# Kernel tuning notes

Hardware: AMD Instinct MI355X
Metric: run time of the kernel (lower is better)

## Reference

```python
import jax, jax.numpy as jnp
import numpy as np

B, L, HEADS, D_HEAD = 2, 2048, 16, 64
D_MODEL = HEADS * D_HEAD            # 1024
D_BI = D_MODEL * 4 // 2             # 2048 (bilinear GLU width)
D_PROJ = D_MODEL * 3 + 2 * D_BI
DEPTH = 0                           # block depth < 2 -> token shift active
NEG_INF = -1e10


def _ln(x, g, b, eps=1e-5):
    m = jnp.mean(x, axis=-1, keepdims=True)
    v = jnp.var(x, axis=-1, keepdims=True)
    return (x - m) * jax.lax.rsqrt(v + eps) * g + b


def _shift(x, n):
    # F.pad(x, (0,0,n,-n)): shift along seq dim by n, zero-fill at front
    return jnp.pad(x, ((0, 0), (n, 0), (0, 0)))[:, : x.shape[1], :]


def setup_inputs() -> dict:
    key = jax.random.key(0)
    ks = jax.random.split(key, 3)
    x = jax.random.normal(ks[0], (B, L, D_MODEL), jnp.float32)
    w_in = jax.random.normal(ks[1], (D_MODEL, D_PROJ), jnp.float32) * (D_MODEL ** -0.5)
    # note: torch init zeros out_proj; we use small random weights so backward is non-trivial
    w_out = jax.random.normal(ks[2], (D_MODEL + D_BI, D_MODEL), jnp.float32) * 0.02
    slopes = jnp.concatenate([2.0 ** jnp.linspace(0.0, -6.0, HEADS // 2),
                              jnp.zeros(HEADS - HEADS // 2)]).astype(jnp.float32)
    return {
        "x": x,
        "in_ln_g": jnp.ones(D_MODEL, jnp.float32), "in_ln_b": jnp.zeros(D_MODEL, jnp.float32),
        "mid_ln_g": jnp.ones(D_PROJ, jnp.float32), "mid_ln_b": jnp.zeros(D_PROJ, jnp.float32),
        "out_ln_g": jnp.ones(D_MODEL, jnp.float32), "out_ln_b": jnp.zeros(D_MODEL, jnp.float32),
        "w_in": w_in, "w_out": w_out, "slopes": slopes,
    }


def reference(x, in_ln_g, in_ln_b, mid_ln_g, mid_ln_b, out_ln_g, out_ln_b, w_in, w_out, slopes):
    b, l, d = x.shape
    x = _ln(x, in_ln_g, in_ln_b)
    if DEPTH < 2:
        x = jnp.concatenate([
            _shift(x[..., : d // 4], 1),
            x[..., d // 4: d - d // 8],
            _shift(x[..., d - d // 8:], 2),
        ], axis=-1)
    h = _ln(x @ w_in, mid_ln_g, mid_ln_b)
    q, k, v, p1, p2 = jnp.split(h, [D_MODEL, 2 * D_MODEL, 3 * D_MODEL, 3 * D_MODEL + D_BI], axis=-1)
    to_heads = lambda t: t.reshape(b, l, HEADS, D_HEAD).transpose(0, 2, 1, 3)  # b h l d
    q, k, v = to_heads(q), to_heads(k), to_heads(v)
    logits = jnp.einsum('bhid,bhjd->bhij', q, k) * (D_HEAD ** -0.5)
    pos = jnp.arange(l)
    alibi = pos[None, None, None, :].astype(logits.dtype) * slopes[None, :, None, None]
    causal = jnp.where(pos[:, None] >= pos[None, :], 0.0, NEG_INF).astype(logits.dtype)
    a = jax.nn.softmax(logits + alibi + causal, axis=-1)
    o = jnp.einsum('bhij,bhjd->bhid', a, v).transpose(0, 2, 1, 3).reshape(b, l, d)
    return _ln(jnp.concatenate([o, p1 * p2], axis=-1) @ w_out, out_ln_g, out_ln_b)
```

## Files before the change

kernel.cpp:

```cpp
#include <hip/hip_runtime.h>

#define B_ 2
#define L_ 2048
#define HEADS_ 16
#define DH_ 64
#define DM_ 1024
#define DBI_ 2048
#define DPROJ_ 7168
#define NTOK (B_*L_)
#define DCAT (DM_ + DBI_)

typedef __bf16 bf16;
typedef __attribute__((ext_vector_type(8))) __bf16 bf16x8;
typedef __attribute__((ext_vector_type(4))) float floatx4;

typedef __attribute__((address_space(1))) const void gptr_t;
typedef __attribute__((address_space(3))) void lptr_t;

__device__ __forceinline__ void g2l16(const void* g, void* l) {
    __builtin_amdgcn_global_load_lds((gptr_t*)g, (lptr_t*)l, 16, 0, 0);
}

__global__ __launch_bounds__(256) void transpose_both(const float* __restrict__ w_in,
                                                      const float* __restrict__ w_out,
                                                      bf16* __restrict__ w_inT,
                                                      bf16* __restrict__ w_outT) {
    __shared__ float tile[32][33];
    int l = blockIdx.x;
    const float* in; bf16* outp; int R, C, bx, by;
    if (l < 7168) { in = w_in;  outp = w_inT;  R = DM_;  C = DPROJ_; bx = l % 224; by = l / 224; }
    else { l -= 7168; in = w_out; outp = w_outT; R = DCAT; C = DM_;   bx = l % 32;  by = l / 32; }
    int c0 = bx * 32, r0 = by * 32;
    int x = threadIdx.x & 31, y = threadIdx.x >> 5;
    for (int i = 0; i < 32; i += 8)
        tile[y + i][x] = in[(size_t)(r0 + y + i) * C + (c0 + x)];
    __syncthreads();
    for (int i = 0; i < 32; i += 8)
        outp[(size_t)(c0 + y + i) * R + (r0 + x)] = (bf16)tile[x][y + i];
}

__global__ __launch_bounds__(256) void ln_shift(const float* __restrict__ x,
                                                const float* __restrict__ g,
                                                const float* __restrict__ bb,
                                                bf16* __restrict__ xs) {
    int tok = blockIdx.x;
    int b = tok / L_, l = tok % L_;
    const float* row = x + (size_t)tok * DM_;
    float vals[4];
    float s = 0.f, s2 = 0.f;
    for (int i = 0; i < 4; i++) {
        float v = row[threadIdx.x + i * 256];
        vals[i] = v; s += v; s2 += v * v;
    }
    __shared__ float red[2][4];
    for (int o = 32; o; o >>= 1) { s += __shfl_xor(s, o); s2 += __shfl_xor(s2, o); }
    int w = threadIdx.x >> 6;
    if ((threadIdx.x & 63) == 0) { red[0][w] = s; red[1][w] = s2; }
    __syncthreads();
    s  = red[0][0] + red[0][1] + red[0][2] + red[0][3];
    s2 = red[1][0] + red[1][1] + red[1][2] + red[1][3];
    float mean = s * (1.f / DM_);
    float var  = s2 * (1.f / DM_) - mean * mean;
    float rstd = rsqrtf(var + 1e-5f);
    for (int i = 0; i < 4; i++) {
        int c = threadIdx.x + i * 256;
        float y = (vals[i] - mean) * rstd * g[c] + bb[c];
        int shift = (c < 256) ? 1 : ((c >= 896) ? 2 : 0);
        int dl = l + shift;
        if (dl < L_) xs[((size_t)b * L_ + dl) * DM_ + c] = (bf16)y;
        if (l == 0 && shift) {
            xs[((size_t)b * L_ + 0) * DM_ + c] = (bf16)0.f;
            if (shift == 2) xs[((size_t)b * L_ + 1) * DM_ + c] = (bf16)0.f;
        }
    }
}

__global__ __launch_bounds__(256, 2) void gemm1_k(const bf16* __restrict__ A,
                                                  const bf16* __restrict__ Bt,
                                                  bf16* __restrict__ C) {
    const int K = DM_, N = DPROJ_;
    int lin = blockIdx.x;
    int chunk = lin >> 7, within = lin & 127;
    int m0 = (within >> 3) * 256;
    int n0 = (chunk * 8 + (within & 7)) * 128;
    __shared__ bf16 As[2][256 * 32];
    __shared__ bf16 Bs[2][128 * 32];
    int t = threadIdx.x, lane = t & 63, wave = t >> 6;
    int c = lane & 15, quad = lane >> 4;
    int wm = wave * 64;
    auto stage = [&](int k0, int bsel) {
        #pragma unroll
        for (int s = 0; s < 4; s++) {
            int f = s * 256 + t;
            int row = f >> 2, kp = (f & 3) * 8;
            g2l16(A + (size_t)(m0 + row) * K + k0 + kp, &As[bsel][f * 8]);
        }
        #pragma unroll
        for (int s = 0; s < 2; s++) {
            int f = s * 256 + t;
            int row = f >> 2, kp = (f & 3) * 8;
            g2l16(Bt + (size_t)(n0 + row) * K + k0 + kp, &Bs[bsel][f * 8]);
        }
    };
    floatx4 acc[4][8] = {};
    stage(0, 0);
    int buf = 0;
    for (int k0 = 0; k0 < K; k0 += 32) {
        __syncthreads();
        if (k0 + 32 < K) stage(k0 + 32, buf ^ 1);
        bf16x8 af[4], bfr[8];
        #pragma unroll
        for (int i = 0; i < 4; i++)
            af[i] = *(const bf16x8*)&As[buf][(wm + i * 16 + c) * 32 + quad * 8];
        #pragma unroll
        for (int j = 0; j < 8; j++)
            bfr[j] = *(const bf16x8*)&Bs[buf][(j * 16 + c) * 32 + quad * 8];
        #pragma unroll
        for (int i = 0; i < 4; i++)
            #pragma unroll
            for (int j = 0; j < 8; j++)
                acc[i][j] = __builtin_amdgcn_mfma_f32_16x16x32_bf16(af[i], bfr[j], acc[i][j], 0, 0, 0);
        buf ^= 1;
    }
    #pragma unroll
    for (int i = 0; i < 4; i++)
        #pragma unroll
        for (int j = 0; j < 8; j++)
            #pragma unroll
            for (int r = 0; r < 4; r++) {
                int row = m0 + wm + i * 16 + quad * 4 + r;
                int col = n0 + j * 16 + c;
                C[(size_t)row * N + col] = (bf16)acc[i][j][r];
            }
}

__global__ __launch_bounds__(256) void gemm2_sk(const bf16* __restrict__ A,
                                                const bf16* __restrict__ Bt,
                                                float* __restrict__ P) {
    const int ldA = DCAT, N = DM_;
    int m0 = blockIdx.x * 128, n0 = blockIdx.y * 128, kz = blockIdx.z;
    const bf16* Ak = A + kz * 1024;
    const bf16* Btk = Bt + kz * 1024;
    float* C = P + (size_t)kz * NTOK * DM_;
    __shared__ bf16 As[2][128 * 32];
    __shared__ bf16 Bs[2][128 * 32];
    int t = threadIdx.x, lane = t & 63, wave = t >> 6;
    int c = lane & 15, quad = lane >> 4;
    int wm = (wave >> 1) * 64, wn = (wave & 1) * 64;
    auto stage = [&](int k0, int bsel) {
        #pragma unroll
        for (int s = 0; s < 2; s++) {
            int f = s * 256 + t;
            int row = f >> 2, kp = (f & 3) * 8;
            g2l16(Ak + (size_t)(m0 + row) * ldA + k0 + kp, &As[bsel][f * 8]);
            g2l16(Btk + (size_t)(n0 + row) * ldA + k0 + kp, &Bs[bsel][f * 8]);
        }
    };
    floatx4 acc[4][4] = {};
    stage(0, 0);
    int buf = 0;
    for (int k0 = 0; k0 < 1024; k0 += 32) {
        __syncthreads();
        if (k0 + 32 < 1024) stage(k0 + 32, buf ^ 1);
        bf16x8 af[4], bfr[4];
        #pragma unroll
        for (int i = 0; i < 4; i++)
            af[i] = *(const bf16x8*)&As[buf][(wm + i * 16 + c) * 32 + quad * 8];
        #pragma unroll
        for (int j = 0; j < 4; j++)
            bfr[j] = *(const bf16x8*)&Bs[buf][(wn + j * 16 + c) * 32 + quad * 8];
        #pragma unroll
        for (int i = 0; i < 4; i++)
            #pragma unroll
            for (int j = 0; j < 4; j++)
                acc[i][j] = __builtin_amdgcn_mfma_f32_16x16x32_bf16(af[i], bfr[j], acc[i][j], 0, 0, 0);
        buf ^= 1;
    }
    #pragma unroll
    for (int i = 0; i < 4; i++)
        #pragma unroll
        for (int j = 0; j < 4; j++)
            #pragma unroll
            for (int r = 0; r < 4; r++) {
                int row = m0 + wm + i * 16 + quad * 4 + r;
                int col = n0 + wn + j * 16 + c;
                C[(size_t)row * N + col] = acc[i][j][r];
            }
}

__global__ __launch_bounds__(256) void mid_ln_fused(const bf16* __restrict__ h,
                                                    const float* __restrict__ g,
                                                    const float* __restrict__ bb,
                                                    bf16* __restrict__ Qp,
                                                    bf16* __restrict__ Kp,
                                                    bf16* __restrict__ Vn,
                                                    bf16* __restrict__ A2) {
    int tok = blockIdx.x;
    int b = tok >> 11, l = tok & 2047;
    size_t base = (size_t)tok * DPROJ_;
    int t = threadIdx.x;
    float v[28];
    float s = 0.f, s2 = 0.f;
    for (int i = 0; i < 28; i++) {
        v[i] = (float)h[base + t + i * 256];
        s += v[i]; s2 += v[i] * v[i];
    }
    __shared__ float red[2][4];
    for (int o = 32; o; o >>= 1) { s += __shfl_xor(s, o); s2 += __shfl_xor(s2, o); }
    int w = t >> 6;
    if ((t & 63) == 0) { red[0][w] = s; red[1][w] = s2; }
    __syncthreads();
    s  = red[0][0] + red[0][1] + red[0][2] + red[0][3];
    s2 = red[1][0] + red[1][1] + red[1][2] + red[1][3];
    float mean = s * (1.f / DPROJ_);
    float var  = s2 * (1.f / DPROJ_) - mean * mean;
    float rstd = rsqrtf(var + 1e-5f);
    #pragma unroll
    for (int i = 0; i < 28; i++) {
        int c = t + i * 256;
        v[i] = (v[i] - mean) * rstd * g[c] + bb[c];
    }
    #pragma unroll
    for (int i = 0; i < 12; i++) {
        int c = t + i * 256;
        int sec = c >> 10;
        int cc = c & 1023;
        int hh = cc >> 6, d = cc & 63;
        size_t idx = (((size_t)b * HEADS_ + hh) * L_ + l) * DH_ + d;
        bf16* dst = (sec == 0) ? Qp : (sec == 1) ? Kp : Vn;
        dst[idx] = (bf16)v[i];
    }
    #pragma unroll
    for (int i = 12; i < 20; i++) {
        int c = t + i * 256;
        A2[(size_t)tok * DCAT + DM_ + (c - 3 * DM_)] = (bf16)(v[i] * v[i + 8]);
    }
}

__global__ __launch_bounds__(256) void vt_pack(const bf16* __restrict__ Vn,
                                               bf16* __restrict__ Vt) {
    __shared__ bf16 tile[32][33];
    int bh = blockIdx.z;
    const bf16* in = Vn + (size_t)bh * L_ * DH_;
    bf16* out = Vt + (size_t)bh * DH_ * L_;
    int l0 = blockIdx.x * 32, d0 = blockIdx.y * 32;
    int x = threadIdx.x & 31, y = threadIdx.x >> 5;
    for (int i = 0; i < 32; i += 8)
        tile[y + i][x] = in[(size_t)(l0 + y + i) * DH_ + d0 + x];
    __syncthreads();
    for (int i = 0; i < 32; i += 8)
        out[(size_t)(d0 + y + i) * L_ + l0 + x] = tile[x][y + i];
}

__global__ __launch_bounds__(256, 4) void attn4(const bf16* __restrict__ Qp,
                                                const bf16* __restrict__ Kp,
                                                const bf16* __restrict__ Vt,
                                                const float* __restrict__ slopes,
                                                bf16* __restrict__ A2) {
    int hd = blockIdx.y, b = blockIdx.z;
    int lin = blockIdx.x + 32 * blockIdx.y + 512 * blockIdx.z;
    int xr = blockIdx.x;
    int qt = ((lin >> 8) & 1) ? (31 - xr) : xr;
    int q0 = qt * 64;
    int t = threadIdx.x, lane = t & 63, wave = t >> 6;
    int quad = lane >> 4, c = lane & 15;
    __shared__ bf16 Ks[2 * 64 * 32];
    __shared__ bf16 Vs[2 * 64 * 32];
    __shared__ bf16 Ps[4][16 * 72];
    int bh = b * HEADS_ + hd;
    const bf16* Qb = Qp + (size_t)bh * L_ * DH_;
    const bf16* Kb = Kp + (size_t)bh * L_ * DH_;
    const bf16* Vb = Vt + (size_t)bh * DH_ * L_;
    const float LOG2E = 1.44269504f;
    float slopeL2 = slopes[hd] * LOG2E;
    const float qscale = 0.125f * LOG2E;

    bf16x8 qf[2];
    int qrow = q0 + wave * 16 + c;
    qf[0] = *(const bf16x8*)(Qb + (size_t)qrow * DH_ + quad * 8);
    qf[1] = *(const bf16x8*)(Qb + (size_t)qrow * DH_ + 32 + quad * 8);
    floatx4 accO[4] = {};
    float lsum[4];
    float mrow[4];
    int i_row0 = q0 + wave * 16 + quad * 4;
    #pragma unroll
    for (int r = 0; r < 4; r++) {
        lsum[r] = 0.f;
        mrow[r] = slopeL2 * (float)(i_row0 + r) + 20.0f;
    }

    int row = t >> 2, kp = (t & 3) * 8;
    bf16* pw = &Ps[wave][0];
    bf16* pwr = pw + (quad * 4) * 72 + c;
    for (int j0 = 0; j0 <= q0; j0 += 64) {
        #pragma unroll
        for (int s = 0; s < 2; s++) {
            g2l16(Kb + (size_t)(j0 + row) * DH_ + s * 32 + kp, &Ks[(s * 256 + t) * 8]);
            g2l16(Vb + (size_t)row * L_ + j0 + s * 32 + kp, &Vs[(s * 256 + t) * 8]);
        }
        __syncthreads();

        bool diag = (j0 == q0);
        #pragma unroll
        for (int nt = 0; nt < 4; nt++) {
            floatx4 sacc = {};
            bf16x8 kf0 = *(const bf16x8*)&Ks[(nt * 16 + c) * 32 + quad * 8];
            bf16x8 kf1 = *(const bf16x8*)&Ks[2048 + (nt * 16 + c) * 32 + quad * 8];
            sacc = __builtin_amdgcn_mfma_f32_16x16x32_bf16(qf[0], kf0, sacc, 0, 0, 0);
            sacc = __builtin_amdgcn_mfma_f32_16x16x32_bf16(qf[1], kf1, sacc, 0, 0, 0);
            int j = j0 + nt * 16 + c;
            float aj = slopeL2 * (float)j;
            #pragma unroll
            for (int r = 0; r < 4; r++) {
                float p = exp2f(fmaf(sacc[r], qscale, aj) - mrow[r]);
                if (diag) p = (j <= i_row0 + r) ? p : 0.f;
                lsum[r] += p;
                pwr[r * 72 + nt * 16] = (bf16)p;
            }
        }
        bf16x8 pf0 = *(const bf16x8*)&pw[c * 72 + quad * 8];
        bf16x8 pf1 = *(const bf16x8*)&pw[c * 72 + 32 + quad * 8];
        #pragma unroll
        for (int nt = 0; nt < 4; nt++) {
            bf16x8 vf0 = *(const bf16x8*)&Vs[(nt * 16 + c) * 32 + quad * 8];
            bf16x8 vf1 = *(const bf16x8*)&Vs[2048 + (nt * 16 + c) * 32 + quad * 8];
            accO[nt] = __builtin_amdgcn_mfma_f32_16x16x32_bf16(pf0, vf0, accO[nt], 0, 0, 0);
            accO[nt] = __builtin_amdgcn_mfma_f32_16x16x32_bf16(pf1, vf1, accO[nt], 0, 0, 0);
        }
        __syncthreads();
    }
    #pragma unroll
    for (int r = 0; r < 4; r++) {
        float l = lsum[r];
        l += __shfl_xor(l, 1);
        l += __shfl_xor(l, 2);
        l += __shfl_xor(l, 4);
        l += __shfl_xor(l, 8);
        lsum[r] = 1.f / l;
    }
    #pragma unroll
    for (int r = 0; r < 4; r++) {
        size_t orow = (size_t)b * L_ + q0 + wave * 16 + quad * 4 + r;
        #pragma unroll
        for (int nt = 0; nt < 4; nt++)
            A2[orow * DCAT + hd * DH_ + nt * 16 + c] = (bf16)(accO[nt][r] * lsum[r]);
    }
}

__global__ __launch_bounds__(256) void out_ln3(const float* __restrict__ P,
                                               const float* __restrict__ g,
                                               const float* __restrict__ bb,
                                               float* __restrict__ out) {
    size_t base = (size_t)blockIdx.x * DM_;
    const size_t stride = (size_t)NTOK * DM_;
    float v[4];
    float s = 0.f, s2 = 0.f;
    for (int i = 0; i < 4; i++) {
        size_t idx = base + threadIdx.x + i * 256;
        v[i] = P[idx] + P[idx + stride] + P[idx + 2 * stride];
        s += v[i]; s2 += v[i] * v[i];
    }
    __shared__ float red[2][4];
    for (int o = 32; o; o >>= 1) { s += __shfl_xor(s, o); s2 += __shfl_xor(s2, o); }
    int w = threadIdx.x >> 6;
    if ((threadIdx.x & 63) == 0) { red[0][w] = s; red[1][w] = s2; }
    __syncthreads();
    s  = red[0][0] + red[0][1] + red[0][2] + red[0][3];
    s2 = red[1][0] + red[1][1] + red[1][2] + red[1][3];
    float mean = s * (1.f / DM_);
    float var  = s2 * (1.f / DM_) - mean * mean;
    float rstd = rsqrtf(var + 1e-5f);
    for (int i = 0; i < 4; i++) {
        int c = threadIdx.x + i * 256;
        out[base + c] = (v[i] - mean) * rstd * g[c] + bb[c];
    }
}

extern "C" void kernel_launch(void* const* d_in, const int* in_sizes, int n_in,
                              void* d_out, int out_size, void* d_ws, size_t ws_size,
                              hipStream_t stream) {
    const float* x     = (const float*)d_in[0];
    const float* in_g  = (const float*)d_in[1];
    const float* in_b  = (const float*)d_in[2];
    const float* mid_g = (const float*)d_in[3];
    const float* mid_b = (const float*)d_in[4];
    const float* out_g = (const float*)d_in[5];
    const float* out_b = (const float*)d_in[6];
    const float* w_in  = (const float*)d_in[7];
    const float* w_out = (const float*)d_in[8];
    const float* slopes = (const float*)d_in[9];
    float* out = (float*)d_out;

    char* ws = (char*)d_ws;
    size_t off = 0;
    auto alloc = [&](size_t n) { char* p = ws + off; off += (n + 255) & ~(size_t)255; return p; };
    bf16* w_inT  = (bf16*)alloc((size_t)DPROJ_ * DM_ * 2);
    bf16* w_outT = (bf16*)alloc((size_t)DM_ * DCAT * 2);
    bf16* xs     = (bf16*)alloc((size_t)NTOK * DM_ * 2);
    bf16* h      = (bf16*)alloc((size_t)NTOK * DPROJ_ * 2);
    bf16* A2     = (bf16*)alloc((size_t)NTOK * DCAT * 2);
    bf16* Qp     = (bf16*)alloc((size_t)NTOK * DM_ * 2);
    bf16* Kp     = (bf16*)alloc((size_t)NTOK * DM_ * 2);
    bf16* Vn     = (bf16*)alloc((size_t)NTOK * DM_ * 2);
    bf16* Vt = xs;
    float* P = (float*)h;

    hipLaunchKernelGGL(transpose_both, dim3(7168 + 3072), dim3(256), 0, stream,
                       w_in, w_out, w_inT, w_outT);
    hipLaunchKernelGGL(ln_shift, dim3(NTOK), dim3(256), 0, stream, x, in_g, in_b, xs);
    hipLaunchKernelGGL(gemm1_k, dim3(896), dim3(256), 0, stream, xs, w_inT, h);
    hipLaunchKernelGGL(mid_ln_fused, dim3(NTOK), dim3(256), 0, stream, h, mid_g, mid_b,
                       Qp, Kp, Vn, A2);
    hipLaunchKernelGGL(vt_pack, dim3(L_ / 32, DH_ / 32, B_ * HEADS_), dim3(256), 0, stream, Vn, Vt);
    hipLaunchKernelGGL(attn4, dim3(32, HEADS_, B_), dim3(256), 0, stream, Qp, Kp, Vt, slopes, A2);
    hipLaunchKernelGGL(gemm2_sk, dim3(NTOK / 128, DM_ / 128, 3), dim3(256), 0, stream,
                       A2, w_outT, P);
    hipLaunchKernelGGL(out_ln3, dim3(NTOK), dim3(256), 0, stream, P, out_g, out_b, out);
}
```

Baseline: 317.3 us.

## Vectorize layernorm kernels and raise GEMM occupancy hints

Rewrites the input, mid and output layernorm kernels to use 16-byte vector loads and stores (float4 / bf16x8) in place of scalar per-element accesses. The mid layernorm kernel remaps threads so each one handles contiguous 8-element chunks, with a split between threads below and above 128 to route Q/K/V and bilinear products. Launch-bound minimum block counts for the two GEMMs are also raised, which pushes the compiler toward fewer registers and risks spills. These changes target memory-bound elementwise kernels and GEMM occupancy.

```diff
diff --git a/kernel.cpp b/kernel.cpp
--- a/kernel.cpp
+++ b/kernel.cpp
@@ -11,6 +11,7 @@
 #define DCAT (DM_ + DBI_)
 
 typedef __bf16 bf16;
+typedef __attribute__((ext_vector_type(4))) __bf16 bf16x4;
 typedef __attribute__((ext_vector_type(8))) __bf16 bf16x8;
 typedef __attribute__((ext_vector_type(4))) float floatx4;
 
@@ -44,38 +45,40 @@
                                                 const float* __restrict__ bb,
                                                 bf16* __restrict__ xs) {
     int tok = blockIdx.x;
-    int b = tok / L_, l = tok % L_;
-    const float* row = x + (size_t)tok * DM_;
-    float vals[4];
-    float s = 0.f, s2 = 0.f;
-    for (int i = 0; i < 4; i++) {
-        float v = row[threadIdx.x + i * 256];
-        vals[i] = v; s += v; s2 += v * v;
-    }
+    int b = tok >> 11, l = tok & 2047;
+    int t = threadIdx.x;
+    float4 v = ((const float4*)(x + (size_t)tok * DM_))[t];
+    float s = v.x + v.y + v.z + v.w;
+    float s2 = v.x * v.x + v.y * v.y + v.z * v.z + v.w * v.w;
     __shared__ float red[2][4];
     for (int o = 32; o; o >>= 1) { s += __shfl_xor(s, o); s2 += __shfl_xor(s2, o); }
-    int w = threadIdx.x >> 6;
-    if ((threadIdx.x & 63) == 0) { red[0][w] = s; red[1][w] = s2; }
+    int w = t >> 6;
+    if ((t & 63) == 0) { red[0][w] = s; red[1][w] = s2; }
     __syncthreads();
     s  = red[0][0] + red[0][1] + red[0][2] + red[0][3];
     s2 = red[1][0] + red[1][1] + red[1][2] + red[1][3];
     float mean = s * (1.f / DM_);
     float var  = s2 * (1.f / DM_) - mean * mean;
     float rstd = rsqrtf(var + 1e-5f);
-    for (int i = 0; i < 4; i++) {
-        int c = threadIdx.x + i * 256;
-        float y = (vals[i] - mean) * rstd * g[c] + bb[c];
-        int shift = (c < 256) ? 1 : ((c >= 896) ? 2 : 0);
-        int dl = l + shift;
-        if (dl < L_) xs[((size_t)b * L_ + dl) * DM_ + c] = (bf16)y;
-        if (l == 0 && shift) {
-            xs[((size_t)b * L_ + 0) * DM_ + c] = (bf16)0.f;
-            if (shift == 2) xs[((size_t)b * L_ + 1) * DM_ + c] = (bf16)0.f;
-        }
-    }
-}
-
-__global__ __launch_bounds__(256, 2) void gemm1_k(const bf16* __restrict__ A,
+    int c = t * 4;
+    float4 gg = ((const float4*)g)[t];
+    float4 bv = ((const float4*)bb)[t];
+    bf16x4 y;
+    y[0] = (bf16)((v.x - mean) * rstd * gg.x + bv.x);
+    y[1] = (bf16)((v.y - mean) * rstd * gg.y + bv.y);
+    y[2] = (bf16)((v.z - mean) * rstd * gg.z + bv.z);
+    y[3] = (bf16)((v.w - mean) * rstd * gg.w + bv.w);
+    int shift = (c < 256) ? 1 : ((c >= 896) ? 2 : 0);
+    int dl = l + shift;
+    if (dl < L_) *(bf16x4*)&xs[((size_t)b * L_ + dl) * DM_ + c] = y;
+    if (l == 0 && shift) {
+        bf16x4 z = {};
+        *(bf16x4*)&xs[((size_t)b * L_) * DM_ + c] = z;
+        if (shift == 2) *(bf16x4*)&xs[((size_t)b * L_ + 1) * DM_ + c] = z;
+    }
+}
+
+__global__ __launch_bounds__(256, 3) void gemm1_k(const bf16* __restrict__ A,
                                                   const bf16* __restrict__ Bt,
                                                   bf16* __restrict__ C) {
     const int K = DM_, N = DPROJ_;
@@ -134,9 +137,9 @@
             }
 }
 
-__global__ __launch_bounds__(256) void gemm2_sk(const bf16* __restrict__ A,
-                                                const bf16* __restrict__ Bt,
-                                                float* __restrict__ P) {
+__global__ __launch_bounds__(256, 4) void gemm2_sk(const bf16* __restrict__ A,
+                                                   const bf16* __restrict__ Bt,
+                                                   float* __restrict__ P) {
     const int ldA = DCAT, N = DM_;
     int m0 = blockIdx.x * 128, n0 = blockIdx.y * 128, kz = blockIdx.z;
     const bf16* Ak = A + kz * 1024;
@@ -197,13 +200,18 @@
                                                     bf16* __restrict__ A2) {
     int tok = blockIdx.x;
     int b = tok >> 11, l = tok & 2047;
-    size_t base = (size_t)tok * DPROJ_;
+    const bf16x8* hrow = (const bf16x8*)(h + (size_t)tok * DPROJ_);
     int t = threadIdx.x;
-    float v[28];
+    int nch = (t < 128) ? 4 : 3;
+    float v[4][8];
     float s = 0.f, s2 = 0.f;
-    for (int i = 0; i < 28; i++) {
-        v[i] = (float)h[base + t + i * 256];
-        s += v[i]; s2 += v[i] * v[i];
+    for (int i = 0; i < nch; i++) {
+        bf16x8 hv = hrow[t + i * 256];
+        #pragma unroll
+        for (int j = 0; j < 8; j++) {
+            float f = (float)hv[j];
+            v[i][j] = f; s += f; s2 += f * f;
+        }
     }
     __shared__ float red[2][4];
     for (int o = 32; o; o >>= 1) { s += __shfl_xor(s, o); s2 += __shfl_xor(s2, o); }
@@ -215,25 +223,40 @@
     float mean = s * (1.f / DPROJ_);
     float var  = s2 * (1.f / DPROJ_) - mean * mean;
     float rstd = rsqrtf(var + 1e-5f);
-    #pragma unroll
-    for (int i = 0; i < 28; i++) {
-        int c = t + i * 256;
-        v[i] = (v[i] - mean) * rstd * g[c] + bb[c];
-    }
-    #pragma unroll
-    for (int i = 0; i < 12; i++) {
-        int c = t + i * 256;
-        int sec = c >> 10;
-        int cc = c & 1023;
+    for (int i = 0; i < nch; i++) {
+        int c = (t + i * 256) * 8;
+        float4 g0 = *(const float4*)&g[c],  g1 = *(const float4*)&g[c + 4];
+        float4 b0 = *(const float4*)&bb[c], b1 = *(const float4*)&bb[c + 4];
+        v[i][0] = (v[i][0] - mean) * rstd * g0.x + b0.x;
+        v[i][1] = (v[i][1] - mean) * rstd * g0.y + b0.y;
+        v[i][2] = (v[i][2] - mean) * rstd * g0.z + b0.z;
+        v[i][3] = (v[i][3] - mean) * rstd * g0.w + b0.w;
+        v[i][4] = (v[i][4] - mean) * rstd * g1.x + b1.x;
+        v[i][5] = (v[i][5] - mean) * rstd * g1.y + b1.y;
+        v[i][6] = (v[i][6] - mean) * rstd * g1.z + b1.z;
+        v[i][7] = (v[i][7] - mean) * rstd * g1.w + b1.w;
+    }
+    bf16x8 o;
+    {
+        int cc = (t < 128) ? t * 8 : (t - 128) * 8;
         int hh = cc >> 6, d = cc & 63;
-        size_t idx = (((size_t)b * HEADS_ + hh) * L_ + l) * DH_ + d;
-        bf16* dst = (sec == 0) ? Qp : (sec == 1) ? Kp : Vn;
-        dst[idx] = (bf16)v[i];
-    }
-    #pragma unroll
-    for (int i = 12; i < 20; i++) {
-        int c = t + i * 256;
-        A2[(size_t)tok * DCAT + DM_ + (c - 3 * DM_)] = (bf16)(v[i] * v[i + 8]);
+        #pragma unroll
+        for (int j = 0; j < 8; j++) o[j] = (bf16)v[0][j];
+        bf16* dst = (t < 128) ? Qp : Kp;
+        *(bf16x8*)&dst[(((size_t)b * HEADS_ + hh) * L_ + l) * DH_ + d] = o;
+    }
+    if (t < 128) {
+        int cc = t * 8, hh = cc >> 6, d = cc & 63;
+        #pragma unroll
+        for (int j = 0; j < 8; j++) o[j] = (bf16)v[1][j];
+        *(bf16x8*)&Vn[(((size_t)b * HEADS_ + hh) * L_ + l) * DH_ + d] = o;
+        #pragma unroll
+        for (int j = 0; j < 8; j++) o[j] = (bf16)(v[2][j] * v[3][j]);
+        *(bf16x8*)&A2[(size_t)tok * DCAT + DM_ + t * 8 + 1024] = o;
+    } else {
+        #pragma unroll
+        for (int j = 0; j < 8; j++) o[j] = (bf16)(v[1][j] * v[2][j]);
+        *(bf16x8*)&A2[(size_t)tok * DCAT + DM_ + (t - 128) * 8] = o;
     }
 }
 
@@ -353,27 +376,33 @@
                                                float* __restrict__ out) {
     size_t base = (size_t)blockIdx.x * DM_;
     const size_t stride = (size_t)NTOK * DM_;
-    float v[4];
-    float s = 0.f, s2 = 0.f;
-    for (int i = 0; i < 4; i++) {
-        size_t idx = base + threadIdx.x + i * 256;
-        v[i] = P[idx] + P[idx + stride] + P[idx + 2 * stride];
-        s += v[i]; s2 += v[i] * v[i];
-    }
+    int t = threadIdx.x;
+    float4 a = *(const float4*)&P[base + t * 4];
+    float4 b1 = *(const float4*)&P[base + stride + t * 4];
+    float4 c1 = *(const float4*)&P[base + 2 * stride + t * 4];
+    float4 v;
+    v.x = a.x + b1.x + c1.x; v.y = a.y + b1.y + c1.y;
+    v.z = a.z + b1.z + c1.z; v.w = a.w + b1.w + c1.w;
+    float s = v.x + v.y + v.z + v.w;
+    float s2 = v.x * v.x + v.y * v.y + v.z * v.z + v.w * v.w;
     __shared__ float red[2][4];
     for (int o = 32; o; o >>= 1) { s += __shfl_xor(s, o); s2 += __shfl_xor(s2, o); }
-    int w = threadIdx.x >> 6;
-    if ((threadIdx.x & 63) == 0) { red[0][w] = s; red[1][w] = s2; }
+    int w = t >> 6;
+    if ((t & 63) == 0) { red[0][w] = s; red[1][w] = s2; }
     __syncthreads();
     s  = red[0][0] + red[0][1] + red[0][2] + red[0][3];
     s2 = red[1][0] + red[1][1] + red[1][2] + red[1][3];
     float mean = s * (1.f / DM_);
     float var  = s2 * (1.f / DM_) - mean * mean;
     float rstd = rsqrtf(var + 1e-5f);
-    for (int i = 0; i < 4; i++) {
-        int c = threadIdx.x + i * 256;
-        out[base + c] = (v[i] - mean) * rstd * g[c] + bb[c];
-    }
+    float4 gg = ((const float4*)g)[t];
+    float4 bv = ((const float4*)bb)[t];
+    float4 y;
+    y.x = (v.x - mean) * rstd * gg.x + bv.x;
+    y.y = (v.y - mean) * rstd * gg.y + bv.y;
+    y.z = (v.z - mean) * rstd * gg.z + bv.z;
+    y.w = (v.w - mean) * rstd * gg.w + bv.w;
+    *(float4*)&out[base + t * 4] = y;
 }
 
 extern "C" void kernel_launch(void* const* d_in, const int* in_sizes, int n_in,
```

Result: slower. 694.4 us (+118.8%).
